# Optimization experiments

Measured on AMD Instinct MI355X. Metric: run time of the kernel, lower is better.

## Reference

```python
import jax, jax.numpy as jnp
import numpy as np

D = 1024  # encoder_output_size

def setup_inputs() -> dict:
    key = jax.random.key(0)
    ks = jax.random.split(key, 5)
    scale = 1.0 / np.sqrt(D)  # roughly matches nn.Linear init spread
    seq = jax.random.normal(ks[0], (2048, 8, D), dtype=jnp.float32)
    Kw1 = jax.random.normal(ks[1], (D, D), dtype=jnp.float32) * scale
    Kw2 = jax.random.normal(ks[2], (D, D), dtype=jnp.float32) * scale
    Qw1 = jax.random.normal(ks[3], (D, D), dtype=jnp.float32) * scale
    Qw2 = jax.random.normal(ks[4], (D, D), dtype=jnp.float32) * scale
    return {"sequence": seq, "Kw1": Kw1, "Kw2": Kw2, "Qw1": Qw1, "Qw2": Qw2}

def _mlp(x, W1, W2):
    # nn.Linear(bias=False): y = x @ W^T ; tanh after each
    return jnp.tanh(jnp.tanh(x @ W1.T) @ W2.T)

def reference(sequence, Kw1, Kw2, Qw1, Qw2):
    x = jnp.transpose(sequence, (1, 0, 2))          # [B, S, D]
    keys = _mlp(x, Kw1, Kw2)                        # [B, S, D]
    queries = _mlp(x, Qw1, Qw2)                     # [B, S, D]
    scale = 1.0 / jnp.sqrt(jnp.float32(x.shape[-1]))
    weights = jnp.einsum('bsd,btd->bst', keys, queries) * scale  # [B, S, S]
    weights = jax.nn.softmax(weights, axis=-1)
    attended = jnp.einsum('bst,btd->bsd', weights, x)            # [B, S, D]
    return jnp.transpose(attended, (1, 0, 2))       # [S, B, D]
```

## Files before the change

### kernel.cpp

```cpp
#include <hip/hip_runtime.h>
#include <hip/hip_bf16.h>

#define SEQ 2048
#define NB 8
#define DIM 1024

typedef __attribute__((ext_vector_type(4))) float f32x4;
typedef __attribute__((ext_vector_type(8))) short bf16x8;
typedef __attribute__((ext_vector_type(4))) unsigned short u16x4;

__device__ __forceinline__ unsigned short f2bf(float f) {
    union { float f; unsigned u; } x; x.f = f;
    unsigned r = x.u + 0x7fffu + ((x.u >> 16) & 1u);
    return (unsigned short)(r >> 16);
}
__device__ __forceinline__ float bf2f(unsigned short u) {
    union { unsigned u; float f; } x; x.u = ((unsigned)u) << 16;
    return x.f;
}

__global__ __launch_bounds__(256) void convert_w4(const float* __restrict__ s0,
                                                  const float* __restrict__ s1,
                                                  const float* __restrict__ s2,
                                                  const float* __restrict__ s3,
                                                  unsigned short* __restrict__ out) {
    int sel = blockIdx.y;
    const float* src = sel < 2 ? (sel == 0 ? s0 : s1) : (sel == 2 ? s2 : s3);
    int i = blockIdx.x * 256 + threadIdx.x;
    float4 v = reinterpret_cast<const float4*>(src)[i];
    u16x4 o = { f2bf(v.x), f2bf(v.y), f2bf(v.z), f2bf(v.w) };
    reinterpret_cast<u16x4*>(out + (size_t)sel * DIM * DIM)[i] = o;
}

__global__ __launch_bounds__(256) void make_xb(const float* __restrict__ seq,
                                               unsigned short* __restrict__ xb) {
    int sb = blockIdx.x;
    int s = sb >> 3, b = sb & 7;
    const float4* src = reinterpret_cast<const float4*>(seq + (size_t)sb * DIM);
    u16x4* dst = reinterpret_cast<u16x4*>(xb + ((size_t)b * SEQ + s) * DIM);
    int t = threadIdx.x;
    float4 v = src[t];
    u16x4 o = { f2bf(v.x), f2bf(v.y), f2bf(v.z), f2bf(v.w) };
    dst[t] = o;
}

__global__ __launch_bounds__(256) void make_xbT(const float* __restrict__ seq,
                                                unsigned short* __restrict__ xbT) {
    __shared__ unsigned short tile[64][65];
    int s0 = blockIdx.x * 64, d0 = blockIdx.y * 64, b = blockIdx.z;
    int t = threadIdx.x;
    int dx = (t & 15) * 4, sy = t >> 4;
    #pragma unroll
    for (int i = 0; i < 4; ++i) {
        int s = s0 + sy + i * 16;
        float4 v = *reinterpret_cast<const float4*>(seq + ((size_t)s * NB + b) * DIM + d0 + dx);
        tile[sy + i * 16][dx + 0] = f2bf(v.x);
        tile[sy + i * 16][dx + 1] = f2bf(v.y);
        tile[sy + i * 16][dx + 2] = f2bf(v.z);
        tile[sy + i * 16][dx + 3] = f2bf(v.w);
    }
    __syncthreads();
    int sx = (t & 15) * 4, dy = t >> 4;
    #pragma unroll
    for (int i = 0; i < 4; ++i) {
        int d = d0 + dy + i * 16;
        u16x4 o = { tile[sx + 0][dy + i * 16], tile[sx + 1][dy + i * 16],
                    tile[sx + 2][dy + i * 16], tile[sx + 3][dy + i * 16] };
        *reinterpret_cast<u16x4*>(xbT + ((size_t)b * DIM + d) * SEQ + s0 + sx) = o;
    }
}

__device__ __forceinline__ void gload16(const unsigned short* g, unsigned short* l) {
    __builtin_amdgcn_global_load_lds((const __attribute__((address_space(1))) void*)g,
                                     (__attribute__((address_space(3))) void*)l,
                                     16, 0, 0);
}

#define MFMA16(I0, J0)                                                                            \
    _Pragma("unroll")                                                                             \
    for (int ks = 0; ks < 2; ++ks)                                                                \
        _Pragma("unroll")                                                                         \
        for (int ii = 0; ii < 4; ++ii)                                                            \
            _Pragma("unroll")                                                                     \
            for (int jj = 0; jj < 2; ++jj)                                                        \
                acc[I0 + ii][J0 + jj] = __builtin_amdgcn_mfma_f32_16x16x32_bf16(                   \
                    a[I0 + ii][ks], b[J0 + jj][ks], acc[I0 + ii][J0 + jj], 0, 0, 0);

template<int MODE>
__global__ __launch_bounds__(512, 2) void gemm256(
    const unsigned short* __restrict__ A, size_t sA,
    const unsigned short* __restrict__ B, size_t sB,
    void* __restrict__ Cv, size_t sC,
    int ldc, int K, float scale)
{
    __shared__ unsigned short AsF[2 * 2 * 8192];
    __shared__ unsigned short BsF[2 * 2 * 8192];

    const int gx = gridDim.x, gy = gridDim.y;
    const int nwg = gx * gy * gridDim.z;
    const int fid = blockIdx.x + gx * (blockIdx.y + gy * blockIdx.z);
    const int cpx = nwg >> 3;
    const int sw = (fid & 7) * cpx + (fid >> 3);
    const int bx = sw % gx;
    const int rem = sw / gx;
    const int by = rem % gy;
    const int bz = rem / gy;

    const unsigned short* Ab = A + sA * bz;
    const unsigned short* Bb = B + sB * bz;
    const int m0 = by * 256;
    const int n0 = bx * 256;

    const int t_ = threadIdx.x;
    const int lane = t_ & 63;
    const int w = t_ >> 6;
    const int wm = w >> 2;
    const int wn = w & 3;

    const int l3 = lane >> 3;
    const int g7 = lane & 7;
    const size_t h128 = (size_t)128 * K;
    const size_t r8 = (size_t)8 * K;
    const unsigned short* gA = Ab + (size_t)(m0 + w * 16 + l3) * K + ((g7 ^ l3) << 3);
    const unsigned short* gB = Bb + (size_t)(n0 + w * 16 + l3) * K + ((g7 ^ l3) << 3);

    const int fr = lane & 15;
    const int hi4 = lane >> 4;
    const int off0 = fr * 64 + (((hi4) ^ g7) << 3);
    const int off1 = fr * 64 + (((4 + hi4) ^ g7) << 3);
    const int bno = (wn & 1) * 4096;
    const int wlds = w * 1024;

    f32x4 acc[8][4] = {};
    const int NT = K >> 6;

    gload16(gA, AsF + wlds);                    gload16(gA + r8, AsF + wlds + 512);
    gload16(gA + h128, AsF + 8192 + wlds);      gload16(gA + h128 + r8, AsF + 8192 + wlds + 512);
    gload16(gB, BsF + wlds);                    gload16(gB + r8, BsF + wlds + 512);
    gload16(gB + h128, BsF + 8192 + wlds);      gload16(gB + h128 + r8, BsF + 8192 + wlds + 512);
    {
        const unsigned short* gb1 = gB + 64;
        gload16(gb1, BsF + 16384 + wlds);               gload16(gb1 + r8, BsF + 16384 + wlds + 512);
        gload16(gb1 + h128, BsF + 16384 + 8192 + wlds); gload16(gb1 + h128 + r8, BsF + 16384 + 8192 + wlds + 512);
    }
    asm volatile("s_waitcnt vmcnt(4)" ::: "memory");
    __builtin_amdgcn_s_barrier();

    const unsigned short* gA1 = gA + 64;
    const unsigned short* gB2 = gB + 128;

    for (int u = 0; u < NT; ++u) {
        const int bu = (u & 1) * 16384;
        const int bn = 16384 - bu;
        const unsigned short* pA = AsF + bu + wm * 8192;
        const unsigned short* pB = BsF + bu + (wn >> 1) * 8192 + bno;
        const bool pfA = (u + 1 < NT);
        const bool pfB = (u + 2 < NT);
        bf16x8 a[8][2], b[4][2];

        #pragma unroll
        for (int i = 0; i < 4; ++i) {
            a[i][0] = *(const bf16x8*)&pA[i * 1024 + off0];
            a[i][1] = *(const bf16x8*)&pA[i * 1024 + off1];
        }
        #pragma unroll
        for (int j = 0; j < 2; ++j) {
            b[j][0] = *(const bf16x8*)&pB[j * 1024 + off0];
            b[j][1] = *(const bf16x8*)&pB[j * 1024 + off1];
        }
        if (pfA) { gload16(gA1, AsF + bn + wlds); gload16(gA1 + r8, AsF + bn + wlds + 512); }
        asm volatile("s_waitcnt lgkmcnt(8)" ::: "memory");
        __builtin_amdgcn_s_barrier();
        asm volatile("s_waitcnt lgkmcnt(0)" ::: "memory");
        __builtin_amdgcn_sched_barrier(0);
        __builtin_amdgcn_s_setprio(1);
        MFMA16(0, 0)
        __builtin_amdgcn_s_setprio(0);
        __builtin_amdgcn_s_barrier();

        #pragma unroll
        for (int j = 2; j < 4; ++j) {
            b[j][0] = *(const bf16x8*)&pB[j * 1024 + off0];
            b[j][1] = *(const bf16x8*)&pB[j * 1024 + off1];
        }
        if (pfA) { gload16(gA1 + h128, AsF + bn + 8192 + wlds); gload16(gA1 + h128 + r8, AsF + bn + 8192 + wlds + 512); }
        __builtin_amdgcn_s_barrier();
        asm volatile("s_waitcnt lgkmcnt(0)" ::: "memory");
        __builtin_amdgcn_sched_barrier(0);
        __builtin_amdgcn_s_setprio(1);
        MFMA16(0, 2)
        __builtin_amdgcn_s_setprio(0);
        __builtin_amdgcn_s_barrier();

        #pragma unroll
        for (int i = 4; i < 8; ++i) {
            a[i][0] = *(const bf16x8*)&pA[i * 1024 + off0];
            a[i][1] = *(const bf16x8*)&pA[i * 1024 + off1];
        }
        if (pfB) { gload16(gB2, BsF + bu + wlds); gload16(gB2 + r8, BsF + bu + wlds + 512); }
        __builtin_amdgcn_s_barrier();
        asm volatile("s_waitcnt lgkmcnt(0)" ::: "memory");
        __builtin_amdgcn_sched_barrier(0);
        __builtin_amdgcn_s_setprio(1);
        MFMA16(4, 0)
        __builtin_amdgcn_s_setprio(0);
        __builtin_amdgcn_s_barrier();

        if (pfB) {
            gload16(gB2 + h128, BsF + bu + 8192 + wlds);
            gload16(gB2 + h128 + r8, BsF + bu + 8192 + wlds + 512);
            asm volatile("s_waitcnt vmcnt(4)" ::: "memory");
        } else {
            asm volatile("s_waitcnt vmcnt(0)" ::: "memory");
        }
        __builtin_amdgcn_s_barrier();
        __builtin_amdgcn_sched_barrier(0);
        __builtin_amdgcn_s_setprio(1);
        MFMA16(4, 2)
        __builtin_amdgcn_s_setprio(0);
        __builtin_amdgcn_s_barrier();

        gA1 += 64; gB2 += 64;
    }

    #pragma unroll
    for (int mi = 0; mi < 8; ++mi)
        #pragma unroll
        for (int ni = 0; ni < 4; ++ni)
            #pragma unroll
            for (int r = 0; r < 4; ++r) {
                int row = m0 + wm * 128 + mi * 16 + hi4 * 4 + r;
                int col = n0 + wn * 64 + ni * 16 + fr;
                if (MODE == 0) {
                    unsigned short* C = reinterpret_cast<unsigned short*>(Cv);
                    C[(size_t)row * ldc + col] = f2bf(tanhf(acc[mi][ni][r]));
                } else if (MODE == 1) {
                    float* C = reinterpret_cast<float*>(Cv) + sC * bz;
                    C[(size_t)row * ldc + col] = acc[mi][ni][r] * scale;
                } else {
                    unsigned short* C = reinterpret_cast<unsigned short*>(Cv) + sC * bz;
                    C[(size_t)row * ldc + col] = f2bf(acc[mi][ni][r] * scale);
                }
            }
}

__global__ __launch_bounds__(256) void softmax_rows_bf16(unsigned short* __restrict__ Z) {
    const size_t row = blockIdx.x;
    unsigned short* z = Z + row * SEQ;
    const int t = threadIdx.x;
    u16x4 v0 = reinterpret_cast<const u16x4*>(z)[2 * t];
    u16x4 v1 = reinterpret_cast<const u16x4*>(z)[2 * t + 1];
    float f[8] = { bf2f(v0[0]), bf2f(v0[1]), bf2f(v0[2]), bf2f(v0[3]),
                   bf2f(v1[0]), bf2f(v1[1]), bf2f(v1[2]), bf2f(v1[3]) };
    float m = f[0];
    #pragma unroll
    for (int j = 1; j < 8; ++j) m = fmaxf(m, f[j]);
    #pragma unroll
    for (int off = 32; off; off >>= 1) m = fmaxf(m, __shfl_xor(m, off, 64));
    __shared__ float redm[4], reds[4];
    const int w = t >> 6, lane = t & 63;
    if (lane == 0) redm[w] = m;
    __syncthreads();
    m = fmaxf(fmaxf(redm[0], redm[1]), fmaxf(redm[2], redm[3]));
    float e[8], s = 0.f;
    #pragma unroll
    for (int j = 0; j < 8; ++j) { e[j] = __expf(f[j] - m); s += e[j]; }
    #pragma unroll
    for (int off = 32; off; off >>= 1) s += __shfl_xor(s, off, 64);
    if (lane == 0) reds[w] = s;
    __syncthreads();
    s = reds[0] + reds[1] + reds[2] + reds[3];
    float inv = 1.0f / s;
    u16x4 o0 = { f2bf(e[0] * inv), f2bf(e[1] * inv), f2bf(e[2] * inv), f2bf(e[3] * inv) };
    u16x4 o1 = { f2bf(e[4] * inv), f2bf(e[5] * inv), f2bf(e[6] * inv), f2bf(e[7] * inv) };
    reinterpret_cast<u16x4*>(z)[2 * t] = o0;
    reinterpret_cast<u16x4*>(z)[2 * t + 1] = o1;
}

extern "C" void kernel_launch(void* const* d_in, const int* in_sizes, int n_in,
                              void* d_out, int out_size, void* d_ws, size_t ws_size,
                              hipStream_t stream) {
    const float* seq  = (const float*)d_in[0];
    const float* Kw1f = (const float*)d_in[1];
    const float* Kw2f = (const float*)d_in[2];
    const float* Qw1f = (const float*)d_in[3];
    const float* Qw2f = (const float*)d_in[4];
    float* out = (float*)d_out;

    char* ws = (char*)d_ws;
    size_t off = 0;
    auto alloc = [&](size_t bytes) { void* p = ws + off; off += bytes; return p; };
    const size_t WBYTES = (size_t)DIM * DIM * 2;
    const size_t XBYTES = (size_t)NB * SEQ * DIM * 2;
    unsigned short* Wk1 = (unsigned short*)alloc(4 * WBYTES);
    unsigned short* Wk2 = Wk1 + (size_t)DIM * DIM;
    unsigned short* Wq1 = Wk2 + (size_t)DIM * DIM;
    unsigned short* Wq2 = Wq1 + (size_t)DIM * DIM;
    unsigned short* xb   = (unsigned short*)alloc(XBYTES);
    unsigned short* hbuf = (unsigned short*)alloc(XBYTES);
    unsigned short* keys = (unsigned short*)alloc(XBYTES);
    unsigned short* P    = (unsigned short*)alloc((size_t)NB * SEQ * SEQ * 2);
    unsigned short* qrs = xb;
    unsigned short* xbT = hbuf;

    convert_w4<<<dim3(DIM * DIM / 4 / 256, 4), 256, 0, stream>>>(Kw1f, Kw2f, Qw1f, Qw2f, Wk1);
    make_xb<<<SEQ * NB, 256, 0, stream>>>(seq, xb);

    dim3 gMLP(DIM / 256, (NB * SEQ) / 256, 1);
    gemm256<0><<<gMLP, 512, 0, stream>>>(xb,   0, Wk1, 0, hbuf, 0, DIM, DIM, 1.0f);
    gemm256<0><<<gMLP, 512, 0, stream>>>(hbuf, 0, Wk2, 0, keys, 0, DIM, DIM, 1.0f);
    gemm256<0><<<gMLP, 512, 0, stream>>>(xb,   0, Wq1, 0, hbuf, 0, DIM, DIM, 1.0f);
    gemm256<0><<<gMLP, 512, 0, stream>>>(hbuf, 0, Wq2, 0, qrs,  0, DIM, DIM, 1.0f);

    dim3 gQK(SEQ / 256, SEQ / 256, NB);
    gemm256<2><<<gQK, 512, 0, stream>>>(keys, (size_t)SEQ * DIM, qrs, (size_t)SEQ * DIM,
                                        P, (size_t)SEQ * SEQ, SEQ, DIM, 0.03125f);

    softmax_rows_bf16<<<NB * SEQ, 256, 0, stream>>>(P);

    make_xbT<<<dim3(SEQ / 64, DIM / 64, NB), 256, 0, stream>>>(seq, xbT);

    dim3 gPV(DIM / 256, SEQ / 256, NB);
    gemm256<1><<<gPV, 512, 0, stream>>>(P, (size_t)SEQ * SEQ, xbT, (size_t)DIM * SEQ,
                                        out, (size_t)DIM, NB * DIM, SEQ, 1.0f);
}
```

Measured before the change: 386.4 us.

## Shrink GEMM tiles from 256x256 to 128x128 with 4-wave workgroups

Replaces the 256x256-tile, 8-wave GEMM with a 128x128-tile, 4-wave version. LDS buffers, the accumulator array, the wave mapping and the interleaving of LDS fragment loads with MFMA groups are all reworked to fit the smaller tile. Launch grids for the MLP, QK and PV GEMMs are adjusted to match. The smaller tile gives more workgroups and less register and LDS pressure per workgroup, which may improve occupancy and load balance, but each tile reuses loaded data less, so global and LDS traffic per flop goes up.

```diff
diff --git a/kernel.cpp b/kernel.cpp
--- a/kernel.cpp
+++ b/kernel.cpp
@@ -76,25 +76,25 @@
                                      16, 0, 0);
 }
 
-#define MFMA16(I0, J0)                                                                            \
+#define MFMA8(I0, J0)                                                                             \
     _Pragma("unroll")                                                                             \
     for (int ks = 0; ks < 2; ++ks)                                                                \
         _Pragma("unroll")                                                                         \
-        for (int ii = 0; ii < 4; ++ii)                                                            \
+        for (int ii = 0; ii < 2; ++ii)                                                            \
             _Pragma("unroll")                                                                     \
             for (int jj = 0; jj < 2; ++jj)                                                        \
                 acc[I0 + ii][J0 + jj] = __builtin_amdgcn_mfma_f32_16x16x32_bf16(                   \
                     a[I0 + ii][ks], b[J0 + jj][ks], acc[I0 + ii][J0 + jj], 0, 0, 0);
 
 template<int MODE>
-__global__ __launch_bounds__(512, 2) void gemm256(
+__global__ __launch_bounds__(256, 2) void gemm128(
     const unsigned short* __restrict__ A, size_t sA,
     const unsigned short* __restrict__ B, size_t sB,
     void* __restrict__ Cv, size_t sC,
     int ldc, int K, float scale)
 {
-    __shared__ unsigned short AsF[2 * 2 * 8192];
-    __shared__ unsigned short BsF[2 * 2 * 8192];
+    __shared__ unsigned short AsF[2 * 2 * 4096];
+    __shared__ unsigned short BsF[2 * 2 * 4096];
 
     const int gx = gridDim.x, gy = gridDim.y;
     const int nwg = gx * gy * gridDim.z;
@@ -108,18 +108,18 @@
 
     const unsigned short* Ab = A + sA * bz;
     const unsigned short* Bb = B + sB * bz;
-    const int m0 = by * 256;
-    const int n0 = bx * 256;
+    const int m0 = by * 128;
+    const int n0 = bx * 128;
 
     const int t_ = threadIdx.x;
     const int lane = t_ & 63;
     const int w = t_ >> 6;
-    const int wm = w >> 2;
-    const int wn = w & 3;
+    const int wm = w >> 1;
+    const int wn = w & 1;
 
     const int l3 = lane >> 3;
     const int g7 = lane & 7;
-    const size_t h128 = (size_t)128 * K;
+    const size_t h64 = (size_t)64 * K;
     const size_t r8 = (size_t)8 * K;
     const unsigned short* gA = Ab + (size_t)(m0 + w * 16 + l3) * K + ((g7 ^ l3) << 3);
     const unsigned short* gB = Bb + (size_t)(n0 + w * 16 + l3) * K + ((g7 ^ l3) << 3);
@@ -128,20 +128,19 @@
     const int hi4 = lane >> 4;
     const int off0 = fr * 64 + (((hi4) ^ g7) << 3);
     const int off1 = fr * 64 + (((4 + hi4) ^ g7) << 3);
-    const int bno = (wn & 1) * 4096;
     const int wlds = w * 1024;
 
-    f32x4 acc[8][4] = {};
+    f32x4 acc[4][4] = {};
     const int NT = K >> 6;
 
-    gload16(gA, AsF + wlds);                    gload16(gA + r8, AsF + wlds + 512);
-    gload16(gA + h128, AsF + 8192 + wlds);      gload16(gA + h128 + r8, AsF + 8192 + wlds + 512);
-    gload16(gB, BsF + wlds);                    gload16(gB + r8, BsF + wlds + 512);
-    gload16(gB + h128, BsF + 8192 + wlds);      gload16(gB + h128 + r8, BsF + 8192 + wlds + 512);
+    gload16(gA, AsF + wlds);                   gload16(gA + r8, AsF + wlds + 512);
+    gload16(gA + h64, AsF + 4096 + wlds);      gload16(gA + h64 + r8, AsF + 4096 + wlds + 512);
+    gload16(gB, BsF + wlds);                   gload16(gB + r8, BsF + wlds + 512);
+    gload16(gB + h64, BsF + 4096 + wlds);      gload16(gB + h64 + r8, BsF + 4096 + wlds + 512);
     {
         const unsigned short* gb1 = gB + 64;
-        gload16(gb1, BsF + 16384 + wlds);               gload16(gb1 + r8, BsF + 16384 + wlds + 512);
-        gload16(gb1 + h128, BsF + 16384 + 8192 + wlds); gload16(gb1 + h128 + r8, BsF + 16384 + 8192 + wlds + 512);
+        gload16(gb1, BsF + 8192 + wlds);              gload16(gb1 + r8, BsF + 8192 + wlds + 512);
+        gload16(gb1 + h64, BsF + 8192 + 4096 + wlds); gload16(gb1 + h64 + r8, BsF + 8192 + 4096 + wlds + 512);
     }
     asm volatile("s_waitcnt vmcnt(4)" ::: "memory");
     __builtin_amdgcn_s_barrier();
@@ -150,65 +149,64 @@
     const unsigned short* gB2 = gB + 128;
 
     for (int u = 0; u < NT; ++u) {
-        const int bu = (u & 1) * 16384;
-        const int bn = 16384 - bu;
-        const unsigned short* pA = AsF + bu + wm * 8192;
-        const unsigned short* pB = BsF + bu + (wn >> 1) * 8192 + bno;
+        const int bu = (u & 1) * 8192;
+        const int bn = 8192 - bu;
+        const unsigned short* pA = AsF + bu + wm * 4096;
+        const unsigned short* pB = BsF + bu + wn * 4096;
         const bool pfA = (u + 1 < NT);
         const bool pfB = (u + 2 < NT);
-        bf16x8 a[8][2], b[4][2];
-
-        #pragma unroll
-        for (int i = 0; i < 4; ++i) {
-            a[i][0] = *(const bf16x8*)&pA[i * 1024 + off0];
-            a[i][1] = *(const bf16x8*)&pA[i * 1024 + off1];
-        }
+        bf16x8 a[4][2], b[4][2];
+
         #pragma unroll
         for (int j = 0; j < 2; ++j) {
             b[j][0] = *(const bf16x8*)&pB[j * 1024 + off0];
             b[j][1] = *(const bf16x8*)&pB[j * 1024 + off1];
         }
+        #pragma unroll
+        for (int i = 0; i < 2; ++i) {
+            a[i][0] = *(const bf16x8*)&pA[i * 1024 + off0];
+            a[i][1] = *(const bf16x8*)&pA[i * 1024 + off1];
+        }
+        #pragma unroll
+        for (int j = 2; j < 4; ++j) {
+            b[j][0] = *(const bf16x8*)&pB[j * 1024 + off0];
+            b[j][1] = *(const bf16x8*)&pB[j * 1024 + off1];
+        }
         if (pfA) { gload16(gA1, AsF + bn + wlds); gload16(gA1 + r8, AsF + bn + wlds + 512); }
-        asm volatile("s_waitcnt lgkmcnt(8)" ::: "memory");
+        asm volatile("s_waitcnt lgkmcnt(4)" ::: "memory");
         __builtin_amdgcn_s_barrier();
         asm volatile("s_waitcnt lgkmcnt(0)" ::: "memory");
         __builtin_amdgcn_sched_barrier(0);
         __builtin_amdgcn_s_setprio(1);
-        MFMA16(0, 0)
+        MFMA8(0, 0)
         __builtin_amdgcn_s_setprio(0);
         __builtin_amdgcn_s_barrier();
 
         #pragma unroll
-        for (int j = 2; j < 4; ++j) {
-            b[j][0] = *(const bf16x8*)&pB[j * 1024 + off0];
-            b[j][1] = *(const bf16x8*)&pB[j * 1024 + off1];
-        }
-        if (pfA) { gload16(gA1 + h128, AsF + bn + 8192 + wlds); gload16(gA1 + h128 + r8, AsF + bn + 8192 + wlds + 512); }
+        for (int i = 2; i < 4; ++i) {
+            a[i][0] = *(const bf16x8*)&pA[i * 1024 + off0];
+            a[i][1] = *(const bf16x8*)&pA[i * 1024 + off1];
+        }
+        if (pfA) { gload16(gA1 + h64, AsF + bn + 4096 + wlds); gload16(gA1 + h64 + r8, AsF + bn + 4096 + wlds + 512); }
         __builtin_amdgcn_s_barrier();
         asm volatile("s_waitcnt lgkmcnt(0)" ::: "memory");
         __builtin_amdgcn_sched_barrier(0);
         __builtin_amdgcn_s_setprio(1);
-        MFMA16(0, 2)
+        MFMA8(2, 0)
         __builtin_amdgcn_s_setprio(0);
         __builtin_amdgcn_s_barrier();
 
-        #pragma unroll
-        for (int i = 4; i < 8; ++i) {
-            a[i][0] = *(const bf16x8*)&pA[i * 1024 + off0];
-            a[i][1] = *(const bf16x8*)&pA[i * 1024 + off1];
-        }
         if (pfB) { gload16(gB2, BsF + bu + wlds); gload16(gB2 + r8, BsF + bu + wlds + 512); }
         __builtin_amdgcn_s_barrier();
-        asm volatile("s_waitcnt lgkmcnt(0)" ::: "memory");
         __builtin_amdgcn_sched_barrier(0);
         __builtin_amdgcn_s_setprio(1);
-        MFMA16(4, 0)
+        MFMA8(2, 2)
         __builtin_amdgcn_s_setprio(0);
         __builtin_amdgcn_s_barrier();
 
         if (pfB) {
-            gload16(gB2 + h128, BsF + bu + 8192 + wlds);
-            gload16(gB2 + h128 + r8, BsF + bu + 8192 + wlds + 512);
+            gload16(gB2 + h64, BsF + bu + 4096 + wlds);
+            gload16(gB2 + h64 + r8, BsF + bu + 4096 + wlds + 512);
             asm volatile("s_waitcnt vmcnt(4)" ::: "memory");
         } else {
             asm volatile("s_waitcnt vmcnt(0)" ::: "memory");
@@ -216,7 +214,7 @@
         __builtin_amdgcn_s_barrier();
         __builtin_amdgcn_sched_barrier(0);
         __builtin_amdgcn_s_setprio(1);
-        MFMA16(4, 2)
+        MFMA8(0, 2)
         __builtin_amdgcn_s_setprio(0);
         __builtin_amdgcn_s_barrier();
 
@@ -224,12 +222,12 @@
     }
 
     #pragma unroll
-    for (int mi = 0; mi < 8; ++mi)
+    for (int mi = 0; mi < 4; ++mi)
         #pragma unroll
         for (int ni = 0; ni < 4; ++ni)
             #pragma unroll
             for (int r = 0; r < 4; ++r) {
-                int row = m0 + wm * 128 + mi * 16 + hi4 * 4 + r;
+                int row = m0 + wm * 64 + mi * 16 + hi4 * 4 + r;
                 int col = n0 + wn * 64 + ni * 16 + fr;
                 if (MODE == 0) {
                     unsigned short* C = reinterpret_cast<unsigned short*>(Cv);
@@ -306,21 +304,21 @@
     convert_w4<<<dim3(DIM * DIM / 4 / 256, 4), 256, 0, stream>>>(Kw1f, Kw2f, Qw1f, Qw2f, Wk1);
     make_xb<<<SEQ * NB, 256, 0, stream>>>(seq, xb);
 
-    dim3 gMLP(DIM / 256, (NB * SEQ) / 256, 1);
-    gemm256<0><<<gMLP, 512, 0, stream>>>(xb,   0, Wk1, 0, hbuf, 0, DIM, DIM, 1.0f);
-    gemm256<0><<<gMLP, 512, 0, stream>>>(hbuf, 0, Wk2, 0, keys, 0, DIM, DIM, 1.0f);
-    gemm256<0><<<gMLP, 512, 0, stream>>>(xb,   0, Wq1, 0, hbuf, 0, DIM, DIM, 1.0f);
-    gemm256<0><<<gMLP, 512, 0, stream>>>(hbuf, 0, Wq2, 0, qrs,  0, DIM, DIM, 1.0f);
-
-    dim3 gQK(SEQ / 256, SEQ / 256, NB);
-    gemm256<2><<<gQK, 512, 0, stream>>>(keys, (size_t)SEQ * DIM, qrs, (size_t)SEQ * DIM,
+    dim3 gMLP(DIM / 128, (NB * SEQ) / 128, 1);
+    gemm128<0><<<gMLP, 256, 0, stream>>>(xb,   0, Wk1, 0, hbuf, 0, DIM, DIM, 1.0f);
+    gemm128<0><<<gMLP, 256, 0, stream>>>(hbuf, 0, Wk2, 0, keys, 0, DIM, DIM, 1.0f);
+    gemm128<0><<<gMLP, 256, 0, stream>>>(xb,   0, Wq1, 0, hbuf, 0, DIM, DIM, 1.0f);
+    gemm128<0><<<gMLP, 256, 0, stream>>>(hbuf, 0, Wq2, 0, qrs,  0, DIM, DIM, 1.0f);
+
+    dim3 gQK(SEQ / 128, SEQ / 128, NB);
+    gemm128<2><<<gQK, 256, 0, stream>>>(keys, (size_t)SEQ * DIM, qrs, (size_t)SEQ * DIM,
                                         P, (size_t)SEQ * SEQ, SEQ, DIM, 0.03125f);
 
     softmax_rows_bf16<<<NB * SEQ, 256, 0, stream>>>(P);
 
     make_xbT<<<dim3(SEQ / 64, DIM / 64, NB), 256, 0, stream>>>(seq, xbT);
 
-    dim3 gPV(DIM / 256, SEQ / 256, NB);
-    gemm256<1><<<gPV, 512, 0, stream>>>(P, (size_t)SEQ * SEQ, xbT, (size_t)DIM * SEQ,
+    dim3 gPV(DIM / 128, SEQ / 128, NB);
+    gemm128<1><<<gPV, 256, 0, stream>>>(P, (size_t)SEQ * SEQ, xbT, (size_t)DIM * SEQ,
                                         out, (size_t)DIM, NB * DIM, SEQ, 1.0f);
 }
```

Result: slower. 436.8 us (+13.0%).

## Fuse softmax into QK/PV GEMM epilogues and batch K/Q MLP GEMMs

Applied to the files above, without the earlier changes.

Removes the separate softmax kernel. The QK GEMM epilogue now writes exp(score*scale) in bf16 and atomically accumulates row sums, and the PV GEMM divides by the row sum. The first-layer K and Q projections are merged into one wider GEMM, and the second-layer projections run as one batched launch, going from four MLP launches to two. The softmax drops max subtraction, which relies on bounded scores: tanh outputs make |score| at most 32. It also adds float atomics, a zero-init kernel and strided-lda GEMM plumbing.

```diff
diff --git a/kernel.cpp b/kernel.cpp
--- a/kernel.cpp
+++ b/kernel.cpp
@@ -19,13 +19,13 @@
     return x.f;
 }
 
-__global__ __launch_bounds__(256) void convert_w4(const float* __restrict__ s0,
-                                                  const float* __restrict__ s1,
-                                                  const float* __restrict__ s2,
-                                                  const float* __restrict__ s3,
+__global__ __launch_bounds__(256) void convert_w4(const float* __restrict__ kw1,
+                                                  const float* __restrict__ kw2,
+                                                  const float* __restrict__ qw1,
+                                                  const float* __restrict__ qw2,
                                                   unsigned short* __restrict__ out) {
     int sel = blockIdx.y;
-    const float* src = sel < 2 ? (sel == 0 ? s0 : s1) : (sel == 2 ? s2 : s3);
+    const float* src = sel == 0 ? kw1 : (sel == 1 ? qw1 : (sel == 2 ? kw2 : qw2));
     int i = blockIdx.x * 256 + threadIdx.x;
     float4 v = reinterpret_cast<const float4*>(src)[i];
     u16x4 o = { f2bf(v.x), f2bf(v.y), f2bf(v.z), f2bf(v.w) };
@@ -70,6 +70,10 @@
     }
 }
 
+__global__ __launch_bounds__(256) void zero_rowsum(float* __restrict__ rs) {
+    rs[blockIdx.x * 256 + threadIdx.x] = 0.0f;
+}
+
 __device__ __forceinline__ void gload16(const unsigned short* g, unsigned short* l) {
     __builtin_amdgcn_global_load_lds((const __attribute__((address_space(1))) void*)g,
                                      (__attribute__((address_space(3))) void*)l,
@@ -88,10 +92,10 @@
 
 template<int MODE>
 __global__ __launch_bounds__(512, 2) void gemm256(
-    const unsigned short* __restrict__ A, size_t sA,
-    const unsigned short* __restrict__ B, size_t sB,
-    void* __restrict__ Cv, size_t sC,
-    int ldc, int K, float scale)
+    const unsigned short* __restrict__ A, size_t sA, int lda,
+    const unsigned short* __restrict__ B, size_t sB, int ldb,
+    void* __restrict__ Cv, size_t sC, int ldc,
+    int K, float scale, float* __restrict__ rowsum)
 {
     __shared__ unsigned short AsF[2 * 2 * 8192];
     __shared__ unsigned short BsF[2 * 2 * 8192];
@@ -119,10 +123,10 @@
 
     const int l3 = lane >> 3;
     const int g7 = lane & 7;
-    const size_t h128 = (size_t)128 * K;
-    const size_t r8 = (size_t)8 * K;
-    const unsigned short* gA = Ab + (size_t)(m0 + w * 16 + l3) * K + ((g7 ^ l3) << 3);
-    const unsigned short* gB = Bb + (size_t)(n0 + w * 16 + l3) * K + ((g7 ^ l3) << 3);
+    const size_t h128a = (size_t)128 * lda, r8a = (size_t)8 * lda;
+    const size_t h128b = (size_t)128 * ldb, r8b = (size_t)8 * ldb;
+    const unsigned short* gA = Ab + (size_t)(m0 + w * 16 + l3) * lda + ((g7 ^ l3) << 3);
+    const unsigned short* gB = Bb + (size_t)(n0 + w * 16 + l3) * ldb + ((g7 ^ l3) << 3);
 
     const int fr = lane & 15;
     const int hi4 = lane >> 4;
@@ -134,14 +138,14 @@
     f32x4 acc[8][4] = {};
     const int NT = K >> 6;
 
-    gload16(gA, AsF + wlds);                    gload16(gA + r8, AsF + wlds + 512);
-    gload16(gA + h128, AsF + 8192 + wlds);      gload16(gA + h128 + r8, AsF + 8192 + wlds + 512);
-    gload16(gB, BsF + wlds);                    gload16(gB + r8, BsF + wlds + 512);
-    gload16(gB + h128, BsF + 8192 + wlds);      gload16(gB + h128 + r8, BsF + 8192 + wlds + 512);
+    gload16(gA, AsF + wlds);                     gload16(gA + r8a, AsF + wlds + 512);
+    gload16(gA + h128a, AsF + 8192 + wlds);      gload16(gA + h128a + r8a, AsF + 8192 + wlds + 512);
+    gload16(gB, BsF + wlds);                     gload16(gB + r8b, BsF + wlds + 512);
+    gload16(gB + h128b, BsF + 8192 + wlds);      gload16(gB + h128b + r8b, BsF + 8192 + wlds + 512);
     {
         const unsigned short* gb1 = gB + 64;
-        gload16(gb1, BsF + 16384 + wlds);               gload16(gb1 + r8, BsF + 16384 + wlds + 512);
-        gload16(gb1 + h128, BsF + 16384 + 8192 + wlds); gload16(gb1 + h128 + r8, BsF + 16384 + 8192 + wlds + 512);
+        gload16(gb1, BsF + 16384 + wlds);                gload16(gb1 + r8b, BsF + 16384 + wlds + 512);
+        gload16(gb1 + h128b, BsF + 16384 + 8192 + wlds); gload16(gb1 + h128b + r8b, BsF + 16384 + 8192 + wlds + 512);
     }
     asm volatile("s_waitcnt vmcnt(4)" ::: "memory");
     __builtin_amdgcn_s_barrier();
@@ -168,7 +172,7 @@
             b[j][0] = *(const bf16x8*)&pB[j * 1024 + off0];
             b[j][1] = *(const bf16x8*)&pB[j * 1024 + off1];
         }
-        if (pfA) { gload16(gA1, AsF + bn + wlds); gload16(gA1 + r8, AsF + bn + wlds + 512); }
+        if (pfA) { gload16(gA1, AsF + bn + wlds); gload16(gA1 + r8a, AsF + bn + wlds + 512); }
         asm volatile("s_waitcnt lgkmcnt(8)" ::: "memory");
         __builtin_amdgcn_s_barrier();
         asm volatile("s_waitcnt lgkmcnt(0)" ::: "memory");
@@ -183,7 +187,7 @@
             b[j][0] = *(const bf16x8*)&pB[j * 1024 + off0];
             b[j][1] = *(const bf16x8*)&pB[j * 1024 + off1];
         }
-        if (pfA) { gload16(gA1 + h128, AsF + bn + 8192 + wlds); gload16(gA1 + h128 + r8, AsF + bn + 8192 + wlds + 512); }
+        if (pfA) { gload16(gA1 + h128a, AsF + bn + 8192 + wlds); gload16(gA1 + h128a + r8a, AsF + bn + 8192 + wlds + 512); }
         __builtin_amdgcn_s_barrier();
         asm volatile("s_waitcnt lgkmcnt(0)" ::: "memory");
         __builtin_amdgcn_sched_barrier(0);
@@ -197,7 +201,7 @@
             a[i][0] = *(const bf16x8*)&pA[i * 1024 + off0];
             a[i][1] = *(const bf16x8*)&pA[i * 1024 + off1];
         }
-        if (pfB) { gload16(gB2, BsF + bu + wlds); gload16(gB2 + r8, BsF + bu + wlds + 512); }
+        if (pfB) { gload16(gB2, BsF + bu + wlds); gload16(gB2 + r8b, BsF + bu + wlds + 512); }
         __builtin_amdgcn_s_barrier();
         asm volatile("s_waitcnt lgkmcnt(0)" ::: "memory");
         __builtin_amdgcn_sched_barrier(0);
@@ -207,8 +211,8 @@
         __builtin_amdgcn_s_barrier();
 
         if (pfB) {
-            gload16(gB2 + h128, BsF + bu + 8192 + wlds);
-            gload16(gB2 + h128 + r8, BsF + bu + 8192 + wlds + 512);
+            gload16(gB2 + h128b, BsF + bu + 8192 + wlds);
+            gload16(gB2 + h128b + r8b, BsF + bu + 8192 + wlds + 512);
             asm volatile("s_waitcnt vmcnt(4)" ::: "memory");
         } else {
             asm volatile("s_waitcnt vmcnt(0)" ::: "memory");
@@ -223,58 +227,53 @@
         gA1 += 64; gB2 += 64;
     }
 
-    #pragma unroll
-    for (int mi = 0; mi < 8; ++mi)
-        #pragma unroll
-        for (int ni = 0; ni < 4; ++ni)
+    if (MODE == 0) {
+        unsigned short* C = reinterpret_cast<unsigned short*>(Cv) + sC * bz;
+        #pragma unroll
+        for (int mi = 0; mi < 8; ++mi)
+            #pragma unroll
+            for (int ni = 0; ni < 4; ++ni)
+                #pragma unroll
+                for (int r = 0; r < 4; ++r) {
+                    int row = m0 + wm * 128 + mi * 16 + hi4 * 4 + r;
+                    int col = n0 + wn * 64 + ni * 16 + fr;
+                    C[(size_t)row * ldc + col] = f2bf(tanhf(acc[mi][ni][r]));
+                }
+    } else if (MODE == 3) {
+        unsigned short* C = reinterpret_cast<unsigned short*>(Cv) + sC * bz;
+        #pragma unroll
+        for (int mi = 0; mi < 8; ++mi)
             #pragma unroll
             for (int r = 0; r < 4; ++r) {
                 int row = m0 + wm * 128 + mi * 16 + hi4 * 4 + r;
-                int col = n0 + wn * 64 + ni * 16 + fr;
-                if (MODE == 0) {
-                    unsigned short* C = reinterpret_cast<unsigned short*>(Cv);
-                    C[(size_t)row * ldc + col] = f2bf(tanhf(acc[mi][ni][r]));
-                } else if (MODE == 1) {
-                    float* C = reinterpret_cast<float*>(Cv) + sC * bz;
-                    C[(size_t)row * ldc + col] = acc[mi][ni][r] * scale;
-                } else {
-                    unsigned short* C = reinterpret_cast<unsigned short*>(Cv) + sC * bz;
-                    C[(size_t)row * ldc + col] = f2bf(acc[mi][ni][r] * scale);
+                float ps = 0.f;
+                #pragma unroll
+                for (int ni = 0; ni < 4; ++ni) {
+                    unsigned short h = f2bf(__expf(acc[mi][ni][r] * scale));
+                    C[(size_t)row * ldc + (n0 + wn * 64 + ni * 16 + fr)] = h;
+                    ps += bf2f(h);
+                }
+                ps += __shfl_xor(ps, 1, 64);
+                ps += __shfl_xor(ps, 2, 64);
+                ps += __shfl_xor(ps, 4, 64);
+                ps += __shfl_xor(ps, 8, 64);
+                if (fr == 0) atomicAdd(&rowsum[(size_t)bz * SEQ + row], ps);
+            }
+    } else {
+        float* C = reinterpret_cast<float*>(Cv) + sC * bz;
+        #pragma unroll
+        for (int mi = 0; mi < 8; ++mi)
+            #pragma unroll
+            for (int r = 0; r < 4; ++r) {
+                int row = m0 + wm * 128 + mi * 16 + hi4 * 4 + r;
+                float invs = 1.0f / rowsum[(size_t)bz * SEQ + row];
+                #pragma unroll
+                for (int ni = 0; ni < 4; ++ni) {
+                    int col = n0 + wn * 64 + ni * 16 + fr;
+                    C[(size_t)row * ldc + col] = acc[mi][ni][r] * invs;
                 }
             }
-}
-
-__global__ __launch_bounds__(256) void softmax_rows_bf16(unsigned short* __restrict__ Z) {
-    const size_t row = blockIdx.x;
-    unsigned short* z = Z + row * SEQ;
-    const int t = threadIdx.x;
-    u16x4 v0 = reinterpret_cast<const u16x4*>(z)[2 * t];
-    u16x4 v1 = reinterpret_cast<const u16x4*>(z)[2 * t + 1];
-    float f[8] = { bf2f(v0[0]), bf2f(v0[1]), bf2f(v0[2]), bf2f(v0[3]),
-                   bf2f(v1[0]), bf2f(v1[1]), bf2f(v1[2]), bf2f(v1[3]) };
-    float m = f[0];
-    #pragma unroll
-    for (int j = 1; j < 8; ++j) m = fmaxf(m, f[j]);
-    #pragma unroll
-    for (int off = 32; off; off >>= 1) m = fmaxf(m, __shfl_xor(m, off, 64));
-    __shared__ float redm[4], reds[4];
-    const int w = t >> 6, lane = t & 63;
-    if (lane == 0) redm[w] = m;
-    __syncthreads();
-    m = fmaxf(fmaxf(redm[0], redm[1]), fmaxf(redm[2], redm[3]));
-    float e[8], s = 0.f;
-    #pragma unroll
-    for (int j = 0; j < 8; ++j) { e[j] = __expf(f[j] - m); s += e[j]; }
-    #pragma unroll
-    for (int off = 32; off; off >>= 1) s += __shfl_xor(s, off, 64);
-    if (lane == 0) reds[w] = s;
-    __syncthreads();
-    s = reds[0] + reds[1] + reds[2] + reds[3];
-    float inv = 1.0f / s;
-    u16x4 o0 = { f2bf(e[0] * inv), f2bf(e[1] * inv), f2bf(e[2] * inv), f2bf(e[3] * inv) };
-    u16x4 o1 = { f2bf(e[4] * inv), f2bf(e[5] * inv), f2bf(e[6] * inv), f2bf(e[7] * inv) };
-    reinterpret_cast<u16x4*>(z)[2 * t] = o0;
-    reinterpret_cast<u16x4*>(z)[2 * t + 1] = o1;
+    }
 }
 
 extern "C" void kernel_launch(void* const* d_in, const int* in_sizes, int n_in,
@@ -288,39 +287,35 @@
     float* out = (float*)d_out;
 
     char* ws = (char*)d_ws;
-    size_t off = 0;
-    auto alloc = [&](size_t bytes) { void* p = ws + off; off += bytes; return p; };
-    const size_t WBYTES = (size_t)DIM * DIM * 2;
-    const size_t XBYTES = (size_t)NB * SEQ * DIM * 2;
-    unsigned short* Wk1 = (unsigned short*)alloc(4 * WBYTES);
-    unsigned short* Wk2 = Wk1 + (size_t)DIM * DIM;
-    unsigned short* Wq1 = Wk2 + (size_t)DIM * DIM;
-    unsigned short* Wq2 = Wq1 + (size_t)DIM * DIM;
-    unsigned short* xb   = (unsigned short*)alloc(XBYTES);
-    unsigned short* hbuf = (unsigned short*)alloc(XBYTES);
-    unsigned short* keys = (unsigned short*)alloc(XBYTES);
-    unsigned short* P    = (unsigned short*)alloc((size_t)NB * SEQ * SEQ * 2);
-    unsigned short* qrs = xb;
-    unsigned short* xbT = hbuf;
-
-    convert_w4<<<dim3(DIM * DIM / 4 / 256, 4), 256, 0, stream>>>(Kw1f, Kw2f, Qw1f, Qw2f, Wk1);
+    const size_t MB = 1024 * 1024;
+    unsigned short* W    = (unsigned short*)(ws);
+    unsigned short* Wkq1 = W;
+    unsigned short* Wk2s = W + 2 * (size_t)DIM * DIM;
+    unsigned short* xb   = (unsigned short*)(ws + 8 * MB);
+    unsigned short* hKQ  = (unsigned short*)(ws + 40 * MB);
+    unsigned short* kq   = (unsigned short*)(ws + 104 * MB);
+    unsigned short* P    = (unsigned short*)(ws + 8 * MB);
+    unsigned short* xbT  = (unsigned short*)(ws + 72 * MB);
+    float* rowsum        = (float*)(ws);
+
+    convert_w4<<<dim3(DIM * DIM / 4 / 256, 4), 256, 0, stream>>>(Kw1f, Kw2f, Qw1f, Qw2f, W);
     make_xb<<<SEQ * NB, 256, 0, stream>>>(seq, xb);
 
-    dim3 gMLP(DIM / 256, (NB * SEQ) / 256, 1);
-    gemm256<0><<<gMLP, 512, 0, stream>>>(xb,   0, Wk1, 0, hbuf, 0, DIM, DIM, 1.0f);
-    gemm256<0><<<gMLP, 512, 0, stream>>>(hbuf, 0, Wk2, 0, keys, 0, DIM, DIM, 1.0f);
-    gemm256<0><<<gMLP, 512, 0, stream>>>(xb,   0, Wq1, 0, hbuf, 0, DIM, DIM, 1.0f);
-    gemm256<0><<<gMLP, 512, 0, stream>>>(hbuf, 0, Wq2, 0, qrs,  0, DIM, DIM, 1.0f);
-
-    dim3 gQK(SEQ / 256, SEQ / 256, NB);
-    gemm256<2><<<gQK, 512, 0, stream>>>(keys, (size_t)SEQ * DIM, qrs, (size_t)SEQ * DIM,
-                                        P, (size_t)SEQ * SEQ, SEQ, DIM, 0.03125f);
-
-    softmax_rows_bf16<<<NB * SEQ, 256, 0, stream>>>(P);
-
+    gemm256<0><<<dim3(2 * DIM / 256, (NB * SEQ) / 256, 1), 512, 0, stream>>>(
+        xb, 0, DIM, Wkq1, 0, DIM, hKQ, 0, 2 * DIM, DIM, 1.0f, nullptr);
+
+    gemm256<0><<<dim3(DIM / 256, (NB * SEQ) / 256, 2), 512, 0, stream>>>(
+        hKQ, (size_t)DIM, 2 * DIM, Wk2s, (size_t)DIM * DIM, DIM,
+        kq, (size_t)NB * SEQ * DIM, DIM, DIM, 1.0f, nullptr);
+
+    zero_rowsum<<<NB * SEQ / 256, 256, 0, stream>>>(rowsum);
     make_xbT<<<dim3(SEQ / 64, DIM / 64, NB), 256, 0, stream>>>(seq, xbT);
 
-    dim3 gPV(DIM / 256, SEQ / 256, NB);
-    gemm256<1><<<gPV, 512, 0, stream>>>(P, (size_t)SEQ * SEQ, xbT, (size_t)DIM * SEQ,
-                                        out, (size_t)DIM, NB * DIM, SEQ, 1.0f);
-}
+    gemm256<3><<<dim3(SEQ / 256, SEQ / 256, NB), 512, 0, stream>>>(
+        kq, (size_t)SEQ * DIM, DIM, kq + (size_t)NB * SEQ * DIM, (size_t)SEQ * DIM, DIM,
+        P, (size_t)SEQ * SEQ, SEQ, DIM, 0.03125f, rowsum);
+
+    gemm256<4><<<dim3(DIM / 256, SEQ / 256, NB), 512, 0, stream>>>(
+        P, (size_t)SEQ * SEQ, SEQ, xbT, (size_t)DIM * SEQ, SEQ,
+        out, (size_t)DIM, NB * DIM, SEQ, 1.0f, rowsum);
+}
```

Result: faster. 369.1 us (-4.5%).
